# Kernel tuning notes

Measured on AMD Instinct MI355X. Metric: run time of the kernel, lower is better.

The kernel has to match this reference:

```python
import jax, jax.numpy as jnp
import numpy as np

ALPHA = 0.5  # mixing weight between dot-product and wedge-norm terms


def setup_inputs() -> dict:
    key = jax.random.key(0)
    kq, kk, kv = jax.random.split(key, 3)
    B, L, H, E = 2, 2048, 8, 32
    queries = jax.random.normal(kq, (B, L, H, E), dtype=jnp.float32)
    keys = jax.random.normal(kk, (B, L, H, E), dtype=jnp.float32)
    values = jax.random.normal(kv, (B, L, H, E), dtype=jnp.float32)
    return {"queries": queries, "keys": keys, "values": values}


def reference(queries, keys, values):
    # queries: [B,L,H,E], keys: [B,S,H,E], values: [B,S,H,D]
    E = queries.shape[-1]
    scale = 1.0 / jnp.sqrt(jnp.asarray(E, dtype=queries.dtype))
    # dot product scores: [B,H,L,S]
    dot = jnp.einsum('blhe,bshe->bhls', queries, keys)
    # squared norms -> broadcastable [B,H,L,1] and [B,H,1,S]
    qn2 = jnp.sum(queries ** 2, axis=-1).transpose(0, 2, 1)[..., :, None]
    kn2 = jnp.sum(keys ** 2, axis=-1).transpose(0, 2, 1)[..., None, :]
    # wedge (Clifford) squared norm, clamped at 0
    wedge = jax.nn.relu(qn2 * kn2 - dot ** 2)
    scores = (ALPHA * dot - (1.0 - ALPHA) * wedge) * scale
    attn = jax.nn.softmax(scores, axis=-1)  # [B,H,L,S]
    # out: [B,L,H,D]
    out = jnp.einsum('bhls,bshd->blhd', attn, values)
    return out
```

## Files before the change

kernel.cpp:

```cpp
#include <hip/hip_runtime.h>
#include <hip/hip_bf16.h>
#include <math.h>


#define NB 2
#define NL 2048
#define NS 2048
#define NH 8
#define NBH 16
#define STRIPS 2
#define NT 16
#define CSC 0.12751742f
#define DEFER_THR 24.0f

#define WS_KN2_OFF 0u
#define WS_KHKL_OFF 131072u
#define WS_VT_OFF (131072u + 4194304u)
#define WS_PACC_OFF (131072u + 4194304u + 2097152u)
#define WS_PML_OFF (WS_PACC_OFF + 8388608u)
#define WS_NEED (WS_PML_OFF + 524288u)

typedef float f32x4 __attribute__((ext_vector_type(4)));
typedef short s16x8 __attribute__((ext_vector_type(8)));
typedef unsigned short u16;

__device__ inline unsigned pk2(float a, float b) {
    __hip_bfloat162 t = __float22bfloat162_rn(make_float2(a, b));
    union { __hip_bfloat162 h; unsigned u; } cv;
    cv.h = t;
    return cv.u;
}
template <int CTRL>
__device__ inline float dpp_add(float x) {
    return x + __int_as_float(__builtin_amdgcn_mov_dpp(__float_as_int(x), CTRL, 0xF, 0xF, false));
}
__device__ inline void dma16(const void* gp, void* lp) {
    __builtin_amdgcn_global_load_lds(
        (__attribute__((address_space(1))) void*)(void*)gp,
        (__attribute__((address_space(3))) void*)lp, 16, 0, 0);
}
__device__ inline void pl32(unsigned& a, unsigned& b) {
    asm("v_permlane32_swap_b32 %0, %1" : "+v"(a), "+v"(b));
}
__device__ inline void pl16(unsigned& a, unsigned& b) {
    asm("v_permlane16_swap_b32 %0, %1" : "+v"(a), "+v"(b));
}
__device__ inline int swzK(int row) { return (row ^ (row >> 2)) & 3; }
__device__ inline int swzV(int row) { return (row + (row >> 3)) & 7; }

__global__ __launch_bounds__(256) void ga_pre(const float* __restrict__ K,
                                              const float* __restrict__ V,
                                              float* __restrict__ kn2w,
                                              u16* __restrict__ khkl,
                                              u16* __restrict__ vtw) {
    __shared__ float Vf[64][36];
    const int T = threadIdx.x;
    const int bh = blockIdx.x >> 5, stile = blockIdx.x & 31;
    const int b = bh >> 3, h = bh & 7;
    const int s0 = stile * 64;
    const int sk = T >> 2, kc = T & 3;

    const float* kp = K + ((size_t)((b * NS + s0 + sk) * NH + h)) * 32 + kc * 8;
    float4 f0 = *(const float4*)kp, f1 = *(const float4*)(kp + 4);
    float kx[8] = {f0.x, f0.y, f0.z, f0.w, f1.x, f1.y, f1.z, f1.w};
    unsigned hh[4], ll[4];
    float kn2p = 0.f;
#pragma unroll
    for (int i = 0; i < 4; i++) {
        float x0 = kx[2 * i], x1 = kx[2 * i + 1];
        kn2p = fmaf(x0, x0, kn2p);
        kn2p = fmaf(x1, x1, kn2p);
        unsigned h01 = pk2(x0, x1);
        hh[i] = h01;
        float h0 = __uint_as_float(h01 << 16);
        float h1 = __uint_as_float(h01 & 0xffff0000u);
        ll[i] = pk2(x0 - h0, x1 - h1);
    }
    u16* kd = khkl + ((size_t)(bh * NS + s0 + sk)) * 64;
    const int swk = sk & 7;
    *(uint4*)(kd + ((kc ^ swk) * 8)) = make_uint4(hh[0], hh[1], hh[2], hh[3]);
    *(uint4*)(kd + (((4 + kc) ^ swk) * 8)) = make_uint4(ll[0], ll[1], ll[2], ll[3]);
    kn2p = dpp_add<0xB1>(kn2p);
    kn2p = dpp_add<0x4E>(kn2p);
    if (kc == 0) kn2w[bh * NS + s0 + sk] = kn2p;

    const float* vp = V + ((size_t)((b * NS + s0 + sk) * NH + h)) * 32 + kc * 8;
    float4 g0 = *(const float4*)vp, g1 = *(const float4*)(vp + 4);
    *(float4*)&Vf[sk][kc * 8] = g0;
    *(float4*)&Vf[sk][kc * 8 + 4] = g1;
    __syncthreads();
    const int dr = T >> 3, c = T & 7;
    float vv[8];
#pragma unroll
    for (int i = 0; i < 8; i++) vv[i] = Vf[c * 8 + i][dr];
    const int phys = c ^ (dr & 7);
    *(uint4*)(vtw + ((size_t)(bh * 32 + dr)) * NS + s0 + phys * 8) =
        make_uint4(pk2(vv[0], vv[1]), pk2(vv[2], vv[3]), pk2(vv[4], vv[5]), pk2(vv[6], vv[7]));
}

__global__ __launch_bounds__(256, 4) void ga_dma(
    const float* __restrict__ Q, const float* __restrict__ kn2w,
    const u16* __restrict__ khkl, const u16* __restrict__ vtw,
    float* __restrict__ pacc, float* __restrict__ pml) {
    __shared__ u16 sK[2][64][64];
    __shared__ u16 sV[2][32][64];

    const int T = threadIdx.x;
    const int lane = T & 63, wave = T >> 6;
    const int g = lane >> 4, lc = lane & 15, g8 = g * 8;
    const int blk = blockIdx.x;
    const int qt = blk & 31, strip = (blk >> 5) & 1, bh = blk >> 6;
    const int b = bh >> 3, h = bh & 7;
    const int qw = qt * 64 + wave * 16;
    const int kb0 = strip * 1024;

    const float* qrow = Q + ((size_t)((b * NL + qw + lc) * NH + h)) * 32 + g8;
    float4 qa = *(const float4*)qrow, qb = *(const float4*)(qrow + 4);
    float q8[8] = {qa.x, qa.y, qa.z, qa.w, qb.x, qb.y, qb.z, qb.w};
    union { unsigned u4[4]; s16x8 v; } qh_, ql_;
    float qn2 = 0.f;
#pragma unroll
    for (int i = 0; i < 4; i++) {
        float x0 = q8[2 * i], x1 = q8[2 * i + 1];
        qn2 = fmaf(x0, x0, qn2);
        qn2 = fmaf(x1, x1, qn2);
        unsigned h01 = pk2(x0, x1);
        qh_.u4[i] = h01;
        float h0 = __uint_as_float(h01 << 16);
        float h1 = __uint_as_float(h01 & 0xffff0000u);
        ql_.u4[i] = pk2(x0 - h0, x1 - h1);
    }
    const s16x8 qh = qh_.v, ql = ql_.v;
    qn2 += __shfl_xor(qn2, 16);
    qn2 += __shfl_xor(qn2, 32);

    const char* ksrc = (const char*)khkl +
        ((size_t)(bh * NS + kb0 + 16 * wave)) * 128 + lane * 16;
    const char* vsrc = (const char*)vtw +
        ((size_t)(bh * 32 + 8 * wave + (lane >> 3))) * (NS * 2) +
        (size_t)(kb0 + (lane & 7) * 8) * 2;
    const float* kn2b = kn2w + (size_t)bh * NS + kb0;

    dma16(ksrc, &sK[0][16 * wave][0]);
    dma16(ksrc + 1024, &sK[0][16 * wave + 8][0]);
    dma16(vsrc, &sV[0][8 * wave][0]);

    f32x4 kn2v[4], kn2n[4];
#pragma unroll
    for (int st = 0; st < 4; st++) kn2v[st] = *(const f32x4*)(kn2b + 16 * st + 4 * g);

    __syncthreads();

    s16x8 ones;
#pragma unroll
    for (int i = 0; i < 8; i++) ones[i] = (short)0x3F80;

    f32x4 acc0 = {0.f, 0.f, 0.f, 0.f}, acc1 = {0.f, 0.f, 0.f, 0.f};
    float m = -1e30f, l = 0.f;
    const f32x4 z = {0.f, 0.f, 0.f, 0.f};
    const int sw = lc & 7;

    for (int t = 0; t < NT; ++t) {
        const int cur = t & 1;
        if (t + 1 < NT) {
            const char* k2 = ksrc + (size_t)(t + 1) * 8192;
            const char* v2 = vsrc + (size_t)(t + 1) * 128;
            dma16(k2, &sK[cur ^ 1][16 * wave][0]);
            dma16(k2 + 1024, &sK[cur ^ 1][16 * wave + 8][0]);
            dma16(v2, &sV[cur ^ 1][8 * wave][0]);
#pragma unroll
            for (int st = 0; st < 4; st++)
                kn2n[st] = *(const f32x4*)(kn2b + (t + 1) * 64 + 16 * st + 4 * g);
        }

        f32x4 d[4];
#pragma unroll
        for (int st = 0; st < 4; st++) {
            s16x8 kh = *(s16x8*)&sK[cur][16 * st + lc][(g ^ sw) * 8];
            s16x8 klo = *(s16x8*)&sK[cur][16 * st + lc][((4 + g) ^ sw) * 8];
            f32x4 dd = __builtin_amdgcn_mfma_f32_16x16x32_bf16(klo, qh, z, 0, 0, 0);
            dd = __builtin_amdgcn_mfma_f32_16x16x32_bf16(kh, ql, dd, 0, 0, 0);
            dd = __builtin_amdgcn_mfma_f32_16x16x32_bf16(kh, qh, dd, 0, 0, 0);
            d[st] = dd;
        }
        s16x8 va0 = *(s16x8*)&sV[cur][lc][(g ^ sw) * 8];
        s16x8 va1 = *(s16x8*)&sV[cur][lc][((4 + g) ^ sw) * 8];
        s16x8 va2 = *(s16x8*)&sV[cur][lc + 16][(g ^ sw) * 8];
        s16x8 va3 = *(s16x8*)&sV[cur][lc + 16][((4 + g) ^ sw) * 8];

        float sc[4][4];
#pragma unroll
        for (int st = 0; st < 4; st++)
#pragma unroll
            for (int r = 0; r < 4; r++) {
                float dd = d[st][r];
                float c = qn2 * kn2v[st][r];
                sc[st][r] = fminf(dd, fmaf(dd, dd, -c) + dd);
            }

        float x0 = fmaxf(fmaxf(sc[0][0], sc[0][1]), fmaxf(sc[0][2], sc[0][3]));
        float x1 = fmaxf(fmaxf(sc[1][0], sc[1][1]), fmaxf(sc[1][2], sc[1][3]));
        float x2 = fmaxf(fmaxf(sc[2][0], sc[2][1]), fmaxf(sc[2][2], sc[2][3]));
        float x3 = fmaxf(fmaxf(sc[3][0], sc[3][1]), fmaxf(sc[3][2], sc[3][3]));
        float tm = fmaxf(fmaxf(x0, x1), fmaxf(x2, x3));
        if (!__all(tm <= m + DEFER_THR)) {
            tm = fmaxf(tm, __shfl_xor(tm, 16));
            tm = fmaxf(tm, __shfl_xor(tm, 32));
            const float nm = fmaxf(m, tm);
            const float al = __builtin_amdgcn_exp2f((m - nm) * CSC);
            m = nm;
            acc0 *= al;
            acc1 *= al;
            l *= al;
        }
        const float negmC = -m * CSC;
        float p[4][4];
#pragma unroll
        for (int st = 0; st < 4; st++)
#pragma unroll
            for (int r = 0; r < 4; r++)
                p[st][r] = __builtin_amdgcn_exp2f(fmaf(sc[st][r], CSC, negmC));

        unsigned w00 = pk2(p[0][0], p[0][1]), w01 = pk2(p[0][2], p[0][3]);
        unsigned w10 = pk2(p[1][0], p[1][1]), w11 = pk2(p[1][2], p[1][3]);
        unsigned w20 = pk2(p[2][0], p[2][1]), w21 = pk2(p[2][2], p[2][3]);
        unsigned w30 = pk2(p[3][0], p[3][1]), w31 = pk2(p[3][2], p[3][3]);
        pl32(w00, w10); pl32(w01, w11);
        pl16(w00, w10); pl16(w01, w11);
        pl32(w20, w30); pl32(w21, w31);
        pl16(w20, w30); pl16(w21, w31);
        union { uint4 u; s16x8 v; } Pb0, Pb1;
        Pb0.u = make_uint4(w00, w01, w10, w11);
        Pb1.u = make_uint4(w20, w21, w30, w31);
        const s16x8 pb0 = Pb0.v, pb1 = Pb1.v;

        acc0 = __builtin_amdgcn_mfma_f32_16x16x32_bf16(va0, pb0, acc0, 0, 0, 0);
        acc0 = __builtin_amdgcn_mfma_f32_16x16x32_bf16(va1, pb1, acc0, 0, 0, 0);
        acc1 = __builtin_amdgcn_mfma_f32_16x16x32_bf16(va2, pb0, acc1, 0, 0, 0);
        acc1 = __builtin_amdgcn_mfma_f32_16x16x32_bf16(va3, pb1, acc1, 0, 0, 0);
        f32x4 lt = __builtin_amdgcn_mfma_f32_16x16x32_bf16(ones, pb0, z, 0, 0, 0);
        lt = __builtin_amdgcn_mfma_f32_16x16x32_bf16(ones, pb1, lt, 0, 0, 0);
        l += lt[0];

        if (t + 1 < NT) {
#pragma unroll
            for (int st = 0; st < 4; st++) kn2v[st] = kn2n[st];
        }
        __syncthreads();
    }

    float* pa = pacc + (((size_t)bh * STRIPS + strip) * NL + (qw + lc)) * 32;
    *(f32x4*)(pa + 4 * g) = acc0;
    *(f32x4*)(pa + 16 + 4 * g) = acc1;
    if (g == 0) {
        *(float2*)(pml + (((size_t)bh * STRIPS + strip) * NL + (qw + lc)) * 2) =
            make_float2(m, l);
    }
}

__global__ __launch_bounds__(256) void ga_combine(const float* __restrict__ pacc,
                                                  const float* __restrict__ pml,
                                                  float* __restrict__ O) {
    const int tid = blockIdx.x * 256 + threadIdx.x;
    const int dq = tid & 7, q = (tid >> 3) & 2047, bh = tid >> 14;
    const int b = bh >> 3, h = bh & 7;
    float2 t0 = *(const float2*)(pml + (((size_t)bh * STRIPS + 0) * NL + q) * 2);
    float2 t1 = *(const float2*)(pml + (((size_t)bh * STRIPS + 1) * NL + q) * 2);
    const float mf = fmaxf(t0.x, t1.x);
    float w0 = __builtin_amdgcn_exp2f((t0.x - mf) * CSC);
    float w1 = __builtin_amdgcn_exp2f((t1.x - mf) * CSC);
    const float inv = 1.f / fmaf(t0.y, w0, t1.y * w1);
    w0 *= inv;
    w1 *= inv;
    const float* pa0 = pacc + (((size_t)bh * STRIPS + 0) * NL + q) * 32 + dq * 4;
    const float* pa1 = pacc + (((size_t)bh * STRIPS + 1) * NL + q) * 32 + dq * 4;
    float4 a0 = *(const float4*)pa0, a1 = *(const float4*)pa1;
    float4 o;
    o.x = fmaf(a0.x, w0, a1.x * w1);
    o.y = fmaf(a0.y, w0, a1.y * w1);
    o.z = fmaf(a0.z, w0, a1.z * w1);
    o.w = fmaf(a0.w, w0, a1.w * w1);
    *(float4*)(O + (((size_t)(b * NL + q)) * NH + h) * 32 + dq * 4) = o;
}

__global__ __launch_bounds__(512, 4) void ga_fallback(
    const float* __restrict__ Q, const float* __restrict__ K,
    const float* __restrict__ V, float* __restrict__ O) {
    __shared__ union {
        struct {
            u16 Kh[2][64][32];
            u16 Kl[2][64][32];
            u16 Vt[2][32][64];
            float kn2[2][64];
        } s;
        struct { float acc[8][32][17]; float m[8][16]; float l[8][16]; } c;
    } u;
    __shared__ u16 sP[8][16][64];

    const int T = threadIdx.x;
    const int lane = T & 63, wave = T >> 6;
    const int g = lane >> 4, lc = lane & 15, g8 = g * 8;
    const int half = wave >> 2;
    const int qt = blockIdx.x & 31;
    const int bh = blockIdx.x >> 5;
    const int b = bh >> 3, h = bh & 7;
    const int qw = qt * 64 + (wave & 3) * 16;

    const float* qrow = Q + ((size_t)((b * NL + qw + lc) * NH + h)) * 32 + g8;
    float4 qa = *(const float4*)qrow, qb = *(const float4*)(qrow + 4);
    float q8[8] = {qa.x, qa.y, qa.z, qa.w, qb.x, qb.y, qb.z, qb.w};
    union { unsigned u4[4]; s16x8 v; } qh_, ql_;
    float qn2 = 0.f;
#pragma unroll
    for (int i = 0; i < 4; i++) {
        float x0 = q8[2 * i], x1 = q8[2 * i + 1];
        qn2 = fmaf(x0, x0, qn2);
        qn2 = fmaf(x1, x1, qn2);
        unsigned h01 = pk2(x0, x1);
        qh_.u4[i] = h01;
        float h0 = __uint_as_float(h01 << 16);
        float h1 = __uint_as_float(h01 & 0xffff0000u);
        ql_.u4[i] = pk2(x0 - h0, x1 - h1);
    }
    const s16x8 qh = qh_.v, ql = ql_.v;
    qn2 += __shfl_xor(qn2, 16);
    qn2 += __shfl_xor(qn2, 32);

    const int Tl = T & 255;
    const int sk = Tl >> 2, kc = Tl & 3;
    const int dv = Tl & 31, vc = Tl >> 5;
    const float* kbase = K + ((size_t)(b * NS * NH) + h) * 32;
    const float* vbase = V + ((size_t)(b * NS * NH) + h) * 32;
    const int kphys = (kc ^ swzK(sk)) * 8;
    const int vphys = (vc ^ swzV(dv)) * 8;

    int s0 = half * 1024;
    float4 ka = *(const float4*)(kbase + (size_t)(s0 + sk) * 256 + kc * 8);
    float4 kb = *(const float4*)(kbase + (size_t)(s0 + sk) * 256 + kc * 8 + 4);
    float vr[8];
#pragma unroll
    for (int i = 0; i < 8; i++) vr[i] = vbase[(size_t)(s0 + 8 * vc + i) * 256 + dv];

    f32x4 acc0 = {0.f, 0.f, 0.f, 0.f}, acc1 = {0.f, 0.f, 0.f, 0.f};
    float m = -INFINITY, l = 0.f;

    for (int t = 0; t < 16; ++t) {
        {
            float kx[8] = {ka.x, ka.y, ka.z, ka.w, kb.x, kb.y, kb.z, kb.w};
            unsigned hh[4], ll[4];
            float kn2p = 0.f;
#pragma unroll
            for (int i = 0; i < 4; i++) {
                float x0 = kx[2 * i], x1 = kx[2 * i + 1];
                kn2p = fmaf(x0, x0, kn2p);
                kn2p = fmaf(x1, x1, kn2p);
                unsigned h01 = pk2(x0, x1);
                hh[i] = h01;
                float h0 = __uint_as_float(h01 << 16);
                float h1 = __uint_as_float(h01 & 0xffff0000u);
                ll[i] = pk2(x0 - h0, x1 - h1);
            }
            *(uint4*)&u.s.Kh[half][sk][kphys] = make_uint4(hh[0], hh[1], hh[2], hh[3]);
            *(uint4*)&u.s.Kl[half][sk][kphys] = make_uint4(ll[0], ll[1], ll[2], ll[3]);
            kn2p = dpp_add<0xB1>(kn2p);
            kn2p = dpp_add<0x4E>(kn2p);
            if (kc == 0) u.s.kn2[half][sk] = kn2p;
            *(uint4*)&u.s.Vt[half][dv][vphys] =
                make_uint4(pk2(vr[0], vr[1]), pk2(vr[2], vr[3]),
                           pk2(vr[4], vr[5]), pk2(vr[6], vr[7]));
        }
        const int tn = (t + 1 < 16) ? t + 1 : t;
        const int sn = half * 1024 + tn * 64;
        ka = *(const float4*)(kbase + (size_t)(sn + sk) * 256 + kc * 8);
        kb = *(const float4*)(kbase + (size_t)(sn + sk) * 256 + kc * 8 + 4);
#pragma unroll
        for (int i = 0; i < 8; i++) vr[i] = vbase[(size_t)(sn + 8 * vc + i) * 256 + dv];

        __syncthreads();

        f32x4 d[4], kn2v[4];
        const f32x4 z = {0.f, 0.f, 0.f, 0.f};
        const int skr = swzK(lc);
#pragma unroll
        for (int st = 0; st < 4; st++) {
            kn2v[st] = *(f32x4*)&u.s.kn2[half][16 * st + 4 * g];
            s16x8 kh = *(s16x8*)&u.s.Kh[half][16 * st + lc][(g ^ skr) * 8];
            s16x8 kl = *(s16x8*)&u.s.Kl[half][16 * st + lc][(g ^ skr) * 8];
            f32x4 dd = __builtin_amdgcn_mfma_f32_16x16x32_bf16(kl, qh, z, 0, 0, 0);
            dd = __builtin_amdgcn_mfma_f32_16x16x32_bf16(kh, ql, dd, 0, 0, 0);
            dd = __builtin_amdgcn_mfma_f32_16x16x32_bf16(kh, qh, dd, 0, 0, 0);
            d[st] = dd;
        }

        float sc[4][4];
#pragma unroll
        for (int st = 0; st < 4; st++)
#pragma unroll
            for (int r = 0; r < 4; r++) {
                float dd = d[st][r];
                float w = fmaxf(fmaf(-dd, dd, qn2 * kn2v[st][r]), 0.f);
                sc[st][r] = (dd - w) * CSC;
            }

        float x0 = fmaxf(fmaxf(sc[0][0], sc[0][1]), fmaxf(sc[0][2], sc[0][3]));
        float x1 = fmaxf(fmaxf(sc[1][0], sc[1][1]), fmaxf(sc[1][2], sc[1][3]));
        float x2 = fmaxf(fmaxf(sc[2][0], sc[2][1]), fmaxf(sc[2][2], sc[2][3]));
        float x3 = fmaxf(fmaxf(sc[3][0], sc[3][1]), fmaxf(sc[3][2], sc[3][3]));
        float tm = fmaxf(fmaxf(x0, x1), fmaxf(x2, x3));
        tm = fmaxf(tm, __shfl_xor(tm, 16));
        tm = fmaxf(tm, __shfl_xor(tm, 32));
        const float nm = fmaxf(m, tm);
        const float al = __builtin_amdgcn_exp2f(m - nm);
        m = nm;
        float p[4][4], ls = 0.f;
#pragma unroll
        for (int st = 0; st < 4; st++)
#pragma unroll
            for (int r = 0; r < 4; r++) {
                p[st][r] = __builtin_amdgcn_exp2f(sc[st][r] - nm);
                ls += p[st][r];
            }
        l = fmaf(l, al, ls);
        acc0 *= al;
        acc1 *= al;

#pragma unroll
        for (int st = 0; st < 4; st++) {
            const int off = ((2 * st + (g >> 1)) ^ (lc & 7)) * 8 + (g & 1) * 4;
            *(uint2*)&sP[wave][lc][off] =
                make_uint2(pk2(p[st][0], p[st][1]), pk2(p[st][2], p[st][3]));
        }
        __builtin_amdgcn_s_waitcnt(0xC07F);

        const int svl = swzV(lc), svh = swzV(lc + 16), spl = lc & 7;
        s16x8 va00 = *(s16x8*)&u.s.Vt[half][lc][(g ^ svl) * 8];
        s16x8 va01 = *(s16x8*)&u.s.Vt[half][lc][((4 + g) ^ svl) * 8];
        s16x8 va10 = *(s16x8*)&u.s.Vt[half][lc + 16][(g ^ svh) * 8];
        s16x8 va11 = *(s16x8*)&u.s.Vt[half][lc + 16][((4 + g) ^ svh) * 8];
        s16x8 pb0 = *(s16x8*)&sP[wave][lc][(g ^ spl) * 8];
        s16x8 pb1 = *(s16x8*)&sP[wave][lc][((4 + g) ^ spl) * 8];
        acc0 = __builtin_amdgcn_mfma_f32_16x16x32_bf16(va00, pb0, acc0, 0, 0, 0);
        acc0 = __builtin_amdgcn_mfma_f32_16x16x32_bf16(va01, pb1, acc0, 0, 0, 0);
        acc1 = __builtin_amdgcn_mfma_f32_16x16x32_bf16(va10, pb0, acc1, 0, 0, 0);
        acc1 = __builtin_amdgcn_mfma_f32_16x16x32_bf16(va11, pb1, acc1, 0, 0, 0);

        __syncthreads();
    }

    l += __shfl_xor(l, 16);
    l += __shfl_xor(l, 32);
#pragma unroll
    for (int r = 0; r < 4; r++) {
        u.c.acc[wave][4 * g + r][lc] = acc0[r];
        u.c.acc[wave][16 + 4 * g + r][lc] = acc1[r];
    }
    if (lane < 16) {
        u.c.m[wave][lc] = m;
        u.c.l[wave][lc] = l;
    }
    __syncthreads();

    const int q = T >> 3, dq = (T & 7) * 4, qr = q & 15;
    const int w0 = q >> 4, w1 = w0 + 4;
    float m0 = u.c.m[w0][qr], m1 = u.c.m[w1][qr];
    float l0 = u.c.l[w0][qr], l1 = u.c.l[w1][qr];
    float mf = fmaxf(m0, m1);
    float e0 = __builtin_amdgcn_exp2f(m0 - mf);
    float e1 = __builtin_amdgcn_exp2f(m1 - mf);
    float inv = 1.f / fmaf(l1, e1, l0 * e0);
    e0 *= inv;
    e1 *= inv;
    float4 o;
    o.x = u.c.acc[w0][dq + 0][qr] * e0 + u.c.acc[w1][dq + 0][qr] * e1;
    o.y = u.c.acc[w0][dq + 1][qr] * e0 + u.c.acc[w1][dq + 1][qr] * e1;
    o.z = u.c.acc[w0][dq + 2][qr] * e0 + u.c.acc[w1][dq + 2][qr] * e1;
    o.w = u.c.acc[w0][dq + 3][qr] * e0 + u.c.acc[w1][dq + 3][qr] * e1;
    *(float4*)(O + ((size_t)((b * NL + qt * 64 + q) * NH + h)) * 32 + dq) = o;
}

extern "C" void kernel_launch(void* const* d_in, const int* in_sizes, int n_in,
                              void* d_out, int out_size, void* d_ws, size_t ws_size,
                              hipStream_t stream) {
    const float* Q = (const float*)d_in[0];
    const float* K = (const float*)d_in[1];
    const float* V = (const float*)d_in[2];
    float* O = (float*)d_out;

    if (ws_size >= (size_t)WS_NEED) {
        float* kn2w = (float*)((char*)d_ws + WS_KN2_OFF);
        u16* khkl = (u16*)((char*)d_ws + WS_KHKL_OFF);
        u16* vtw = (u16*)((char*)d_ws + WS_VT_OFF);
        float* pacc = (float*)((char*)d_ws + WS_PACC_OFF);
        float* pml = (float*)((char*)d_ws + WS_PML_OFF);
        ga_pre<<<NBH * 32, 256, 0, stream>>>(K, V, kn2w, khkl, vtw);
        ga_dma<<<NBH * 32 * STRIPS, 256, 0, stream>>>(Q, kn2w, khkl, vtw, pacc, pml);
        ga_combine<<<(NBH * NL * 8) / 256, 256, 0, stream>>>(pacc, pml, O);
    } else {
        ga_fallback<<<NBH * 32, 512, 0, stream>>>(Q, K, V, O);
    }
}
```

Measured before the change: 105.1 us.

## Software-pipeline QK MFMA one tile ahead of softmax/PV in attention loop

Restructures the main attention loop so the QK^T MFMAs for tile i are issued before the softmax and PV of tile i-1, with a prologue and epilogue, so matrix-core work overlaps the exp/VALU work. Row-sum accumulation now stays in an MFMA accumulator instead of a per-tile scalar add, and the score and exponent math is written with packed float2 vectors. The launch-bounds occupancy hint drops from 4 to 3 blocks to leave room for the extra live registers. The V transpose in shared memory of the prep kernel is XOR-swizzled to reduce bank conflicts. The cost is higher register pressure and lower occupancy.

```diff
diff --git a/kernel.cpp b/kernel.cpp
--- a/kernel.cpp
+++ b/kernel.cpp
@@ -21,6 +21,7 @@
 #define WS_NEED (WS_PML_OFF + 524288u)
 
 typedef float f32x4 __attribute__((ext_vector_type(4)));
+typedef float f32x2 __attribute__((ext_vector_type(2)));
 typedef short s16x8 __attribute__((ext_vector_type(8)));
 typedef unsigned short u16;
 
@@ -86,19 +87,21 @@
 
     const float* vp = V + ((size_t)((b * NS + s0 + sk) * NH + h)) * 32 + kc * 8;
     float4 g0 = *(const float4*)vp, g1 = *(const float4*)(vp + 4);
-    *(float4*)&Vf[sk][kc * 8] = g0;
-    *(float4*)&Vf[sk][kc * 8 + 4] = g1;
+    const int chv = kc ^ ((sk >> 3) & 3);
+    *(float4*)&Vf[sk][chv * 8] = g0;
+    *(float4*)&Vf[sk][chv * 8 + 4] = g1;
     __syncthreads();
     const int dr = T >> 3, c = T & 7;
     float vv[8];
 #pragma unroll
-    for (int i = 0; i < 8; i++) vv[i] = Vf[c * 8 + i][dr];
+    for (int i = 0; i < 8; i++)
+        vv[i] = Vf[c * 8 + i][(((dr >> 3) ^ (c & 3)) << 3) + (dr & 7)];
     const int phys = c ^ (dr & 7);
     *(uint4*)(vtw + ((size_t)(bh * 32 + dr)) * NS + s0 + phys * 8) =
         make_uint4(pk2(vv[0], vv[1]), pk2(vv[2], vv[3]), pk2(vv[4], vv[5]), pk2(vv[6], vv[7]));
 }
 
-__global__ __launch_bounds__(256, 4) void ga_dma(
+__global__ __launch_bounds__(256, 3) void ga_dma(
     const float* __restrict__ Q, const float* __restrict__ kn2w,
     const u16* __restrict__ khkl, const u16* __restrict__ vtw,
     float* __restrict__ pacc, float* __restrict__ pml) {
@@ -144,11 +147,6 @@
     dma16(ksrc, &sK[0][16 * wave][0]);
     dma16(ksrc + 1024, &sK[0][16 * wave + 8][0]);
     dma16(vsrc, &sV[0][8 * wave][0]);
-
-    f32x4 kn2v[4], kn2n[4];
-#pragma unroll
-    for (int st = 0; st < 4; st++) kn2v[st] = *(const f32x4*)(kn2b + 16 * st + 4 * g);
-
     __syncthreads();
 
     s16x8 ones;
@@ -156,53 +154,53 @@
     for (int i = 0; i < 8; i++) ones[i] = (short)0x3F80;
 
     f32x4 acc0 = {0.f, 0.f, 0.f, 0.f}, acc1 = {0.f, 0.f, 0.f, 0.f};
-    float m = -1e30f, l = 0.f;
+    f32x4 lacc = {0.f, 0.f, 0.f, 0.f};
+    float m = -1e30f;
     const f32x4 z = {0.f, 0.f, 0.f, 0.f};
     const int sw = lc & 7;
 
-    for (int t = 0; t < NT; ++t) {
-        const int cur = t & 1;
-        if (t + 1 < NT) {
-            const char* k2 = ksrc + (size_t)(t + 1) * 8192;
-            const char* v2 = vsrc + (size_t)(t + 1) * 128;
-            dma16(k2, &sK[cur ^ 1][16 * wave][0]);
-            dma16(k2 + 1024, &sK[cur ^ 1][16 * wave + 8][0]);
-            dma16(v2, &sV[cur ^ 1][8 * wave][0]);
-#pragma unroll
-            for (int st = 0; st < 4; st++)
-                kn2n[st] = *(const f32x4*)(kn2b + (t + 1) * 64 + 16 * st + 4 * g);
-        }
-
-        f32x4 d[4];
+    f32x4 d_p[4], kn2_p[4];
+    s16x8 va_p[4];
+
+    auto frags_qk = [&](int buf, f32x4* dc) {
 #pragma unroll
         for (int st = 0; st < 4; st++) {
-            s16x8 kh = *(s16x8*)&sK[cur][16 * st + lc][(g ^ sw) * 8];
-            s16x8 klo = *(s16x8*)&sK[cur][16 * st + lc][((4 + g) ^ sw) * 8];
+            s16x8 kh = *(s16x8*)&sK[buf][16 * st + lc][(g ^ sw) * 8];
+            s16x8 klo = *(s16x8*)&sK[buf][16 * st + lc][((4 + g) ^ sw) * 8];
             f32x4 dd = __builtin_amdgcn_mfma_f32_16x16x32_bf16(klo, qh, z, 0, 0, 0);
             dd = __builtin_amdgcn_mfma_f32_16x16x32_bf16(kh, ql, dd, 0, 0, 0);
             dd = __builtin_amdgcn_mfma_f32_16x16x32_bf16(kh, qh, dd, 0, 0, 0);
-            d[st] = dd;
-        }
-        s16x8 va0 = *(s16x8*)&sV[cur][lc][(g ^ sw) * 8];
-        s16x8 va1 = *(s16x8*)&sV[cur][lc][((4 + g) ^ sw) * 8];
-        s16x8 va2 = *(s16x8*)&sV[cur][lc + 16][(g ^ sw) * 8];
-        s16x8 va3 = *(s16x8*)&sV[cur][lc + 16][((4 + g) ^ sw) * 8];
-
+            dc[st] = dd;
+        }
+    };
+    auto load_v = [&](int buf, s16x8* va) {
+        va[0] = *(s16x8*)&sV[buf][lc][(g ^ sw) * 8];
+        va[1] = *(s16x8*)&sV[buf][lc][((4 + g) ^ sw) * 8];
+        va[2] = *(s16x8*)&sV[buf][lc + 16][(g ^ sw) * 8];
+        va[3] = *(s16x8*)&sV[buf][lc + 16][((4 + g) ^ sw) * 8];
+    };
+    auto softmax_pv = [&](const f32x4* dp, const f32x4* kn2p, const s16x8* vap) {
+        const f32x2 qn2v = {qn2, qn2};
         float sc[4][4];
 #pragma unroll
-        for (int st = 0; st < 4; st++)
-#pragma unroll
-            for (int r = 0; r < 4; r++) {
-                float dd = d[st][r];
-                float c = qn2 * kn2v[st][r];
-                sc[st][r] = fminf(dd, fmaf(dd, dd, -c) + dd);
-            }
-
-        float x0 = fmaxf(fmaxf(sc[0][0], sc[0][1]), fmaxf(sc[0][2], sc[0][3]));
-        float x1 = fmaxf(fmaxf(sc[1][0], sc[1][1]), fmaxf(sc[1][2], sc[1][3]));
-        float x2 = fmaxf(fmaxf(sc[2][0], sc[2][1]), fmaxf(sc[2][2], sc[2][3]));
-        float x3 = fmaxf(fmaxf(sc[3][0], sc[3][1]), fmaxf(sc[3][2], sc[3][3]));
-        float tm = fmaxf(fmaxf(x0, x1), fmaxf(x2, x3));
+        for (int st = 0; st < 4; st++) {
+            f32x2 dd0 = {dp[st][0], dp[st][1]}, dd1 = {dp[st][2], dp[st][3]};
+            f32x2 kk0 = {kn2p[st][0], kn2p[st][1]}, kk1 = {kn2p[st][2], kn2p[st][3]};
+            f32x2 e0 = dd0 - qn2v * kk0;
+            f32x2 e1 = dd1 - qn2v * kk1;
+            f32x2 t0 = dd0 * dd0 + e0;
+            f32x2 t1 = dd1 * dd1 + e1;
+            sc[st][0] = fminf(dp[st][0], t0[0]);
+            sc[st][1] = fminf(dp[st][1], t0[1]);
+            sc[st][2] = fminf(dp[st][2], t1[0]);
+            sc[st][3] = fminf(dp[st][3], t1[1]);
+        }
+        float a0 = fmaxf(fmaxf(sc[0][0], sc[0][1]), sc[0][2]);
+        float a1 = fmaxf(fmaxf(sc[0][3], sc[1][0]), sc[1][1]);
+        float a2 = fmaxf(fmaxf(sc[1][2], sc[1][3]), sc[2][0]);
+        float a3 = fmaxf(fmaxf(sc[2][1], sc[2][2]), sc[2][3]);
+        float a4 = fmaxf(fmaxf(sc[3][0], sc[3][1]), sc[3][2]);
+        float tm = fmaxf(fmaxf(fmaxf(a0, a1), fmaxf(a2, a3)), fmaxf(a4, sc[3][3]));
         if (!__all(tm <= m + DEFER_THR)) {
             tm = fmaxf(tm, __shfl_xor(tm, 16));
             tm = fmaxf(tm, __shfl_xor(tm, 32));
@@ -211,16 +209,21 @@
             m = nm;
             acc0 *= al;
             acc1 *= al;
-            l *= al;
+            lacc *= al;
         }
         const float negmC = -m * CSC;
+        const f32x2 cscv = {CSC, CSC}, nmv = {negmC, negmC};
         float p[4][4];
 #pragma unroll
-        for (int st = 0; st < 4; st++)
-#pragma unroll
-            for (int r = 0; r < 4; r++)
-                p[st][r] = __builtin_amdgcn_exp2f(fmaf(sc[st][r], CSC, negmC));
-
+        for (int st = 0; st < 4; st++) {
+            f32x2 s0 = {sc[st][0], sc[st][1]}, s1 = {sc[st][2], sc[st][3]};
+            f32x2 e0 = s0 * cscv + nmv;
+            f32x2 e1 = s1 * cscv + nmv;
+            p[st][0] = __builtin_amdgcn_exp2f(e0[0]);
+            p[st][1] = __builtin_amdgcn_exp2f(e0[1]);
+            p[st][2] = __builtin_amdgcn_exp2f(e1[0]);
+            p[st][3] = __builtin_amdgcn_exp2f(e1[1]);
+        }
         unsigned w00 = pk2(p[0][0], p[0][1]), w01 = pk2(p[0][2], p[0][3]);
         unsigned w10 = pk2(p[1][0], p[1][1]), w11 = pk2(p[1][2], p[1][3]);
         unsigned w20 = pk2(p[2][0], p[2][1]), w21 = pk2(p[2][2], p[2][3]);
@@ -233,22 +236,55 @@
         Pb0.u = make_uint4(w00, w01, w10, w11);
         Pb1.u = make_uint4(w20, w21, w30, w31);
         const s16x8 pb0 = Pb0.v, pb1 = Pb1.v;
-
-        acc0 = __builtin_amdgcn_mfma_f32_16x16x32_bf16(va0, pb0, acc0, 0, 0, 0);
-        acc0 = __builtin_amdgcn_mfma_f32_16x16x32_bf16(va1, pb1, acc0, 0, 0, 0);
-        acc1 = __builtin_amdgcn_mfma_f32_16x16x32_bf16(va2, pb0, acc1, 0, 0, 0);
-        acc1 = __builtin_amdgcn_mfma_f32_16x16x32_bf16(va3, pb1, acc1, 0, 0, 0);
-        f32x4 lt = __builtin_amdgcn_mfma_f32_16x16x32_bf16(ones, pb0, z, 0, 0, 0);
-        lt = __builtin_amdgcn_mfma_f32_16x16x32_bf16(ones, pb1, lt, 0, 0, 0);
-        l += lt[0];
-
-        if (t + 1 < NT) {
-#pragma unroll
-            for (int st = 0; st < 4; st++) kn2v[st] = kn2n[st];
-        }
+        acc0 = __builtin_amdgcn_mfma_f32_16x16x32_bf16(vap[0], pb0, acc0, 0, 0, 0);
+        acc0 = __builtin_amdgcn_mfma_f32_16x16x32_bf16(vap[1], pb1, acc0, 0, 0, 0);
+        acc1 = __builtin_amdgcn_mfma_f32_16x16x32_bf16(vap[2], pb0, acc1, 0, 0, 0);
+        acc1 = __builtin_amdgcn_mfma_f32_16x16x32_bf16(vap[3], pb1, acc1, 0, 0, 0);
+        lacc = __builtin_amdgcn_mfma_f32_16x16x32_bf16(ones, pb0, lacc, 0, 0, 0);
+        lacc = __builtin_amdgcn_mfma_f32_16x16x32_bf16(ones, pb1, lacc, 0, 0, 0);
+    };
+
+    {
+        dma16(ksrc + 8192, &sK[1][16 * wave][0]);
+        dma16(ksrc + 8192 + 1024, &sK[1][16 * wave + 8][0]);
+        dma16(vsrc + 128, &sV[1][8 * wave][0]);
+        frags_qk(0, d_p);
+#pragma unroll
+        for (int st = 0; st < 4; st++)
+            kn2_p[st] = *(const f32x4*)(kn2b + 16 * st + 4 * g);
+        load_v(0, va_p);
         __syncthreads();
     }
 
+#pragma unroll 2
+    for (int i = 1; i < NT; ++i) {
+        const int cur = i & 1;
+        if (i + 1 < NT) {
+            const char* k2 = ksrc + (size_t)(i + 1) * 8192;
+            const char* v2 = vsrc + (size_t)(i + 1) * 128;
+            dma16(k2, &sK[cur ^ 1][16 * wave][0]);
+            dma16(k2 + 1024, &sK[cur ^ 1][16 * wave + 8][0]);
+            dma16(v2, &sV[cur ^ 1][8 * wave][0]);
+        }
+        f32x4 d_c[4], kn2_c[4];
+        frags_qk(cur, d_c);
+#pragma unroll
+        for (int st = 0; st < 4; st++)
+            kn2_c[st] = *(const f32x4*)(kn2b + i * 64 + 16 * st + 4 * g);
+        softmax_pv(d_p, kn2_p, va_p);
+        s16x8 va_c[4];
+        load_v(cur, va_c);
+#pragma unroll
+        for (int st = 0; st < 4; st++) {
+            d_p[st] = d_c[st];
+            kn2_p[st] = kn2_c[st];
+            va_p[st] = va_c[st];
+        }
+        if (i + 1 < NT) __syncthreads();
+    }
+    softmax_pv(d_p, kn2_p, va_p);
+
+    const float l = lacc[0];
     float* pa = pacc + (((size_t)bh * STRIPS + strip) * NL + (qw + lc)) * 32;
     *(f32x4*)(pa + 4 * g) = acc0;
     *(f32x4*)(pa + 16 + 4 * g) = acc1;
```

New measurement: 106.4 us. About the same (+1.1%).
